# Performance work log

Measured on AMD Instinct MI355X. Metric: run time of the kernel, lower is better.

The kernel has to match this reference:

```python
import jax, jax.numpy as jnp
import numpy as np

N_NODES = 50
VOCAB = 21128
EPS = 1e-8


def _gcn(x, edge_index, W, b):
    # x: [N,128], edge_index: [2,E] (src,dst). PyG GCNConv with self-loops and
    # symmetric normalization: out = D^-1/2 (A+I) D^-1/2 (x W) + b
    N = x.shape[0]
    loops = jnp.arange(N, dtype=edge_index.dtype)
    src = jnp.concatenate([edge_index[0], loops])
    dst = jnp.concatenate([edge_index[1], loops])
    xw = x @ W  # [N,10]
    deg = jax.ops.segment_sum(jnp.ones(src.shape[0], x.dtype), dst, num_segments=N)
    dinv = jnp.where(deg > 0, jax.lax.rsqrt(deg), 0.0)
    norm = dinv[src] * dinv[dst]  # [E+N]
    out = jax.ops.segment_sum(norm[:, None] * xw[src], dst, num_segments=N)
    return out + b


def _mp_match(self_feat, cross_feat, assign_w, w1, b1, w2, b2):
    # cosine similarity along feature dim (torch dim=1), eps-clamped norms
    a = assign_w * self_feat   # [50,10]
    c = assign_w * cross_feat  # [50,10]
    dot = jnp.sum(a * c, axis=1)
    na = jnp.maximum(jnp.linalg.norm(a, axis=1), EPS)
    nc = jnp.maximum(jnp.linalg.norm(c, axis=1), EPS)
    dist = dot / (na * nc)  # [50]
    h = jnp.concatenate([dist[:, None], self_feat], axis=-1)  # [50,11]
    h = jax.nn.relu(h @ w1 + b1) @ w2 + b2  # [50,20]
    return h


def _forward_one(emb_table, conv_w, conv_b, cross_w, attn_coef, assign_w,
                 mp_w1, mp_b1, mp_w2, mp_b2, ffn_w1, ffn_b1, ffn_w2, ffn_b2,
                 u_tok, r_tok, u_edge, r_edge):
    u_emb = emb_table[u_tok]  # [50,128]
    r_emb = emb_table[r_tok]
    u_self = _gcn(u_emb, u_edge, conv_w, conv_b)  # [50,10]
    r_self = _gcn(r_emb, r_edge, conv_w, conv_b)
    u_cross = attn_coef @ (r_emb @ cross_w)  # [50,10]
    r_cross = attn_coef @ (u_emb @ cross_w)
    hu = _mp_match(u_self, u_cross, assign_w, mp_w1, mp_b1, mp_w2, mp_b2)
    hr = _mp_match(r_self, r_cross, assign_w, mp_w1, mp_b1, mp_w2, mp_b2)
    g_u = jnp.max(hu, axis=0)  # [20]
    g_r = jnp.max(hr, axis=0)
    feat = jnp.concatenate([g_u, g_r, g_u * g_r, jnp.abs(g_u - g_r)], axis=-1)  # [80]
    logits = jax.nn.relu(feat @ ffn_w1 + ffn_b1) @ ffn_w2 + ffn_b2  # [1]
    return jax.nn.sigmoid(logits)


def setup_inputs() -> dict:
    key = jax.random.key(0)
    ks = jax.random.split(key, 20)
    B, E, D = 4096, 256, 128
    inp = {
        'utterance_input': jax.random.randint(ks[0], (B, N_NODES), 0, VOCAB, dtype=jnp.int32),
        'response_input': jax.random.randint(ks[1], (B, N_NODES), 0, VOCAB, dtype=jnp.int32),
        'utterance_graph_adj': jax.random.randint(ks[2], (B, 2, E), 0, N_NODES, dtype=jnp.int32),
        'response_graph_adj': jax.random.randint(ks[3], (B, 2, E), 0, N_NODES, dtype=jnp.int32),
        'emb_table': jax.random.normal(ks[4], (VOCAB, D), jnp.float32) * 0.02,
        'conv_w': jax.random.normal(ks[5], (D, 10), jnp.float32) * 0.1,
        'conv_b': jnp.zeros((10,), jnp.float32),
        'cross_w': jax.random.uniform(ks[6], (D, 10), jnp.float32),
        'attn_coef': jax.random.uniform(ks[7], (N_NODES, N_NODES), jnp.float32),
        'assign_w': jax.random.uniform(ks[8], (N_NODES, 10), jnp.float32),
        'mp_w1': jax.random.normal(ks[9], (11, 20), jnp.float32) * 0.3,
        'mp_b1': jnp.zeros((20,), jnp.float32),
        'mp_w2': jax.random.normal(ks[10], (20, 20), jnp.float32) * 0.2,
        'mp_b2': jnp.zeros((20,), jnp.float32),
        'ffn_w1': jax.random.normal(ks[11], (80, 40), jnp.float32) * 0.1,
        'ffn_b1': jnp.zeros((40,), jnp.float32),
        'ffn_w2': jax.random.normal(ks[12], (40, 1), jnp.float32) * 0.1,
        'ffn_b2': jnp.zeros((1,), jnp.float32),
    }
    return inp


def reference(utterance_input, response_input, utterance_graph_adj, response_graph_adj,
              emb_table, conv_w, conv_b, cross_w, attn_coef, assign_w,
              mp_w1, mp_b1, mp_w2, mp_b2, ffn_w1, ffn_b1, ffn_w2, ffn_b2):
    f = jax.vmap(_forward_one,
                 in_axes=(None,) * 14 + (0, 0, 0, 0))
    return f(emb_table, conv_w, conv_b, cross_w, attn_coef, assign_w,
             mp_w1, mp_b1, mp_w2, mp_b2, ffn_w1, ffn_b1, ffn_w2, ffn_b2,
             utterance_input, response_input, utterance_graph_adj, response_graph_adj)  # [B,1]
```

## Files before the change

kernel.cpp:

```cpp
#include <hip/hip_runtime.h>
#include <math.h>

#define NN 50
#define XS 12
#define AWW 13

__global__ __launch_bounds__(256) void precompute_proj(
    const float* __restrict__ emb,
    const float* __restrict__ conv_w,
    const float* __restrict__ cross_w,
    const float* __restrict__ attn,
    float* __restrict__ emb_proj,
    float* __restrict__ attn_t,
    int nrows)
{
    if (blockIdx.x == 0) {
        for (int i = threadIdx.x; i < NN * NN; i += 256) {
            int k = i / NN, r = i % NN;
            attn_t[k * NN + r] = attn[r * NN + k];
        }
    }
    const int lane = threadIdx.x & 63;
    const int w    = threadIdx.x >> 6;
    const int r    = blockIdx.x * 64 + lane;
    if (r >= nrows) return;

    const float* wb = (w < 2) ? conv_w : cross_w;
    const int j0 = (w & 1) * 5;

    float acc[5] = {0.0f, 0.0f, 0.0f, 0.0f, 0.0f};
    const float4* rp = (const float4*)(emb + (size_t)r * 128);
#pragma unroll
    for (int q = 0; q < 32; ++q) {
        float4 v = rp[q];
        const float xs[4] = { v.x, v.y, v.z, v.w };
#pragma unroll
        for (int t = 0; t < 4; ++t) {
            const int k = 4 * q + t;
#pragma unroll
            for (int jj = 0; jj < 5; ++jj)
                acc[jj] += xs[t] * wb[k * 10 + j0 + jj];
        }
    }
    float* op = emb_proj + (size_t)r * 20 + w * 5;
#pragma unroll
    for (int jj = 0; jj < 5; ++jj) op[jj] = acc[jj];
}

__global__ __launch_bounds__(128, 8) void gmn_fused(
    const int* __restrict__ tok_u_all, const int* __restrict__ tok_r_all,
    const int* __restrict__ adj_u_all, const int* __restrict__ adj_r_all,
    const float* __restrict__ emb_proj,
    const float* __restrict__ attn_t,
    const float* __restrict__ conv_b,
    const float* __restrict__ assign_w,
    const float* __restrict__ mp_w1, const float* __restrict__ mp_b1,
    const float* __restrict__ mp_w2, const float* __restrict__ mp_b2,
    const float* __restrict__ ffn_w1, const float* __restrict__ ffn_b1,
    const float* __restrict__ ffn_w2, const float* __restrict__ ffn_b2,
    float* __restrict__ out, int E)
{
    const int b    = blockIdx.x;
    const int tid  = threadIdx.x;
    const int lane = tid & 63;
    const int g    = tid >> 6;

    __shared__ __attribute__((aligned(16))) unsigned s_A[2][NN * AWW];
    __shared__ __attribute__((aligned(16))) float    s_buf[2][NN * XS];
    __shared__ __attribute__((aligned(16))) float    s_g2[2][24];

    for (int i = lane; i < NN * AWW; i += 64) s_A[g][i] = 0u;

    float rx[10];
#pragma unroll
    for (int j = 0; j < 10; ++j) rx[j] = 0.0f;

    if (lane < NN) {
        const int t = (g ? tok_r_all : tok_u_all)[(size_t)b * NN + lane];
        const float4* p = (const float4*)(emb_proj + (size_t)t * 20);
        float4 v0 = p[0], v1 = p[1], v2 = p[2], v3 = p[3], v4 = p[4];
        rx[0] = v0.x; rx[1] = v0.y; rx[2] = v0.z; rx[3] = v0.w;
        rx[4] = v1.x; rx[5] = v1.y; rx[6] = v1.z; rx[7] = v1.w;
        rx[8] = v2.x; rx[9] = v2.y;
        float* ci = &s_buf[g][lane * XS];
        *(float4*)(ci)     = make_float4(v2.z, v2.w, v3.x, v3.y);
        *(float4*)(ci + 4) = make_float4(v3.z, v3.w, v4.x, v4.y);
        *(float2*)(ci + 8) = make_float2(v4.z, v4.w);
    }
    {
        const int* adj = (g ? adj_r_all : adj_u_all) + (size_t)b * 2 * E;
        for (int e = lane; e < E; e += 64) {
            int src = adj[e], dst = adj[E + e];
            atomicAdd(&s_A[g][dst * AWW + (src >> 2)], 1u << ((src & 3) * 8));
        }
    }
    __syncthreads();

    float di = 0.0f;
    float cr[10];
#pragma unroll
    for (int j = 0; j < 10; ++j) cr[j] = 0.0f;

    if (lane < NN) {
        unsigned s = 0;
#pragma unroll
        for (int kw = 0; kw < AWW; ++kw) {
            unsigned a = s_A[g][lane * AWW + kw];
            s += (a & 0xFFu) + ((a >> 8) & 0xFFu) + ((a >> 16) & 0xFFu) + (a >> 24);
        }
        di = rsqrtf(1.0f + (float)s);
#pragma unroll
        for (int j = 0; j < 10; ++j) rx[j] *= di;

        const int i = lane;
        const float* cio = s_buf[g ^ 1];
#pragma unroll 10
        for (int k = 0; k < NN; ++k) {
            float aik = attn_t[k * NN + i];
            const float* crow = &cio[k * XS];
            float4 c0 = *(const float4*)crow;
            float4 c1 = *(const float4*)(crow + 4);
            float2 c2 = *(const float2*)(crow + 8);
            cr[0] += aik * c0.x; cr[1] += aik * c0.y;
            cr[2] += aik * c0.z; cr[3] += aik * c0.w;
            cr[4] += aik * c1.x; cr[5] += aik * c1.y;
            cr[6] += aik * c1.z; cr[7] += aik * c1.w;
            cr[8] += aik * c2.x; cr[9] += aik * c2.y;
        }
    }
    __syncthreads();

    if (lane < NN) {
        float* x = &s_buf[g][lane * XS];
        *(float4*)(x)     = make_float4(rx[0], rx[1], rx[2], rx[3]);
        *(float4*)(x + 4) = make_float4(rx[4], rx[5], rx[6], rx[7]);
        *(float2*)(x + 8) = make_float2(rx[8], rx[9]);
    }
    __builtin_amdgcn_wave_barrier();

    float sf[10];
    float h1[20];

    if (lane < NN) {
        const int i = lane;
        float acc[10];
#pragma unroll
        for (int j = 0; j < 10; ++j) acc[j] = rx[j];
#pragma unroll
        for (int kw = 0; kw < 12; ++kw) {
            unsigned a = s_A[g][i * AWW + kw];
            float cc[4] = { (float)(a & 0xFFu), (float)((a >> 8) & 0xFFu),
                            (float)((a >> 16) & 0xFFu), (float)(a >> 24) };
            const float* x0 = &s_buf[g][(4 * kw) * XS];
#pragma unroll
            for (int t = 0; t < 4; ++t) {
                const float c = cc[t];
                const float* xr = x0 + t * XS;
                float4 p0 = *(const float4*)xr;
                float4 p1 = *(const float4*)(xr + 4);
                float2 p2 = *(const float2*)(xr + 8);
                acc[0] += c * p0.x; acc[1] += c * p0.y;
                acc[2] += c * p0.z; acc[3] += c * p0.w;
                acc[4] += c * p1.x; acc[5] += c * p1.y;
                acc[6] += c * p1.z; acc[7] += c * p1.w;
                acc[8] += c * p2.x; acc[9] += c * p2.y;
            }
        }
        {
            unsigned a = s_A[g][i * AWW + 12];
            float cc[2] = { (float)(a & 0xFFu), (float)((a >> 8) & 0xFFu) };
            const float* x0 = &s_buf[g][48 * XS];
#pragma unroll
            for (int t = 0; t < 2; ++t) {
                const float c = cc[t];
                const float* xr = x0 + t * XS;
                float4 p0 = *(const float4*)xr;
                float4 p1 = *(const float4*)(xr + 4);
                float2 p2 = *(const float2*)(xr + 8);
                acc[0] += c * p0.x; acc[1] += c * p0.y;
                acc[2] += c * p0.z; acc[3] += c * p0.w;
                acc[4] += c * p1.x; acc[5] += c * p1.y;
                acc[6] += c * p1.z; acc[7] += c * p1.w;
                acc[8] += c * p2.x; acc[9] += c * p2.y;
            }
        }
#pragma unroll
        for (int j = 0; j < 10; ++j) sf[j] = di * acc[j] + conv_b[j];

        float dot = 0.0f, na2 = 0.0f, nc2 = 0.0f;
        const float2* awp = (const float2*)(assign_w + i * 10);
#pragma unroll
        for (int q = 0; q < 5; ++q) {
            float2 wv = awp[q];
            float a0 = wv.x * sf[2 * q],     d0 = wv.x * cr[2 * q];
            float a1 = wv.y * sf[2 * q + 1], d1 = wv.y * cr[2 * q + 1];
            dot += a0 * d0 + a1 * d1;
            na2 += a0 * a0 + a1 * a1;
            nc2 += d0 * d0 + d1 * d1;
        }
        float dist = dot / (fmaxf(sqrtf(na2), 1e-8f) * fmaxf(sqrtf(nc2), 1e-8f));

#pragma unroll
        for (int o = 0; o < 20; ++o) {
            float t = mp_b1[o] + dist * mp_w1[o];
#pragma unroll
            for (int j = 0; j < 10; ++j) t += sf[j] * mp_w1[(1 + j) * 20 + o];
            h1[o] = fmaxf(t, 0.0f);
        }
    }

#pragma unroll
    for (int o = 0; o < 20; ++o) {
        float v = -INFINITY;
        if (lane < NN) {
            float t = mp_b2[o];
#pragma unroll
            for (int q = 0; q < 20; ++q) t += h1[q] * mp_w2[q * 20 + o];
            v = t;
        }
        v = fmaxf(v, __shfl_xor(v, 1));
        v = fmaxf(v, __shfl_xor(v, 2));
        v = fmaxf(v, __shfl_xor(v, 4));
        v = fmaxf(v, __shfl_xor(v, 8));
        v = fmaxf(v, __shfl_xor(v, 16));
        v = fmaxf(v, __shfl_xor(v, 32));
        if (lane == 0) s_g2[g][o] = v;
    }
    __syncthreads();

    if (g == 0) {
        float p = 0.0f;
        if (lane < 40) {
            float acc = ffn_b1[lane];
#pragma unroll
            for (int i = 0; i < 20; ++i) {
                float gu = s_g2[0][i], gr = s_g2[1][i];
                acc += gu * ffn_w1[i * 40 + lane]
                     + gr * ffn_w1[(20 + i) * 40 + lane]
                     + gu * gr * ffn_w1[(40 + i) * 40 + lane]
                     + fabsf(gu - gr) * ffn_w1[(60 + i) * 40 + lane];
            }
            p = fmaxf(acc, 0.0f) * ffn_w2[lane];
        }
        p += __shfl_xor(p, 1);  p += __shfl_xor(p, 2);  p += __shfl_xor(p, 4);
        p += __shfl_xor(p, 8);  p += __shfl_xor(p, 16); p += __shfl_xor(p, 32);
        if (lane == 0)
            out[b] = 1.0f / (1.0f + expf(-(p + ffn_b2[0])));
    }
}

extern "C" void kernel_launch(void* const* d_in, const int* in_sizes, int n_in,
                              void* d_out, int out_size, void* d_ws, size_t ws_size,
                              hipStream_t stream)
{
    const int*   tok_u    = (const int*)d_in[0];
    const int*   tok_r    = (const int*)d_in[1];
    const int*   adj_u    = (const int*)d_in[2];
    const int*   adj_r    = (const int*)d_in[3];
    const float* emb      = (const float*)d_in[4];
    const float* conv_w   = (const float*)d_in[5];
    const float* conv_b   = (const float*)d_in[6];
    const float* cross_w  = (const float*)d_in[7];
    const float* attn     = (const float*)d_in[8];
    const float* assign_w = (const float*)d_in[9];
    const float* mp_w1    = (const float*)d_in[10];
    const float* mp_b1    = (const float*)d_in[11];
    const float* mp_w2    = (const float*)d_in[12];
    const float* mp_b2    = (const float*)d_in[13];
    const float* ffn_w1   = (const float*)d_in[14];
    const float* ffn_b1   = (const float*)d_in[15];
    const float* ffn_w2   = (const float*)d_in[16];
    const float* ffn_b2   = (const float*)d_in[17];

    const int B     = in_sizes[0] / 50;
    const int E     = in_sizes[2] / (2 * B);
    const int nrows = in_sizes[4] / 128;

    float* emb_proj = (float*)d_ws;
    float* attn_t   = emb_proj + (size_t)nrows * 20;

    precompute_proj<<<(nrows + 63) / 64, 256, 0, stream>>>(
        emb, conv_w, cross_w, attn, emb_proj, attn_t, nrows);

    gmn_fused<<<B, 128, 0, stream>>>(
        tok_u, tok_r, adj_u, adj_r, emb_proj, attn_t, conv_b,
        assign_w, mp_w1, mp_b1, mp_w2, mp_b2,
        ffn_w1, ffn_b1, ffn_w2, ffn_b2,
        (float*)d_out, E);
}
```

Baseline: 191.1 us.

## Broadcast node features with readlane instead of LDS and drop a barrier

The cross-attention matmul and the GCN neighbour aggregation now broadcast each node's feature row from registers with amdgcn readlane, instead of staging rows in shared memory and reading them back. Each wave computes the cross features from its own embeddings and writes them into the other wave's shared slot. It also reads its adjacency row right after its own atomics, without a block barrier. This cuts LDS traffic and one of the two __syncthreads, at the cost of scalar readlane instructions and more VGPRs. It also relies on ordering of LDS operations within a single wave.

```diff
diff --git a/kernel.cpp b/kernel.cpp
--- a/kernel.cpp
+++ b/kernel.cpp
@@ -4,6 +4,10 @@
 #define NN 50
 #define XS 12
 #define AWW 13
+
+__device__ __forceinline__ float rlane(float v, int k) {
+    return __uint_as_float(__builtin_amdgcn_readlane(__float_as_uint(v), (unsigned)k));
+}
 
 __global__ __launch_bounds__(256) void precompute_proj(
     const float* __restrict__ emb,
@@ -66,14 +70,14 @@
     const int g    = tid >> 6;
 
     __shared__ __attribute__((aligned(16))) unsigned s_A[2][NN * AWW];
-    __shared__ __attribute__((aligned(16))) float    s_buf[2][NN * XS];
+    __shared__ __attribute__((aligned(16))) float    s_x[2][NN * XS];
     __shared__ __attribute__((aligned(16))) float    s_g2[2][24];
 
     for (int i = lane; i < NN * AWW; i += 64) s_A[g][i] = 0u;
 
-    float rx[10];
-#pragma unroll
-    for (int j = 0; j < 10; ++j) rx[j] = 0.0f;
+    float rx[10], ci[10];
+#pragma unroll
+    for (int j = 0; j < 10; ++j) { rx[j] = 0.0f; ci[j] = 0.0f; }
 
     if (lane < NN) {
         const int t = (g ? tok_r_all : tok_u_all)[(size_t)b * NN + lane];
@@ -82,10 +86,9 @@
         rx[0] = v0.x; rx[1] = v0.y; rx[2] = v0.z; rx[3] = v0.w;
         rx[4] = v1.x; rx[5] = v1.y; rx[6] = v1.z; rx[7] = v1.w;
         rx[8] = v2.x; rx[9] = v2.y;
-        float* ci = &s_buf[g][lane * XS];
-        *(float4*)(ci)     = make_float4(v2.z, v2.w, v3.x, v3.y);
-        *(float4*)(ci + 4) = make_float4(v3.z, v3.w, v4.x, v4.y);
-        *(float2*)(ci + 8) = make_float2(v4.z, v4.w);
+        ci[0] = v2.z; ci[1] = v2.w; ci[2] = v3.x; ci[3] = v3.y;
+        ci[4] = v3.z; ci[5] = v3.w; ci[6] = v4.x; ci[7] = v4.y;
+        ci[8] = v4.z; ci[9] = v4.w;
     }
     {
         const int* adj = (g ? adj_r_all : adj_u_all) + (size_t)b * 2 * E;
@@ -94,98 +97,70 @@
             atomicAdd(&s_A[g][dst * AWW + (src >> 2)], 1u << ((src & 3) * 8));
         }
     }
-    __syncthreads();
-
-    float di = 0.0f;
-    float cr[10];
-#pragma unroll
-    for (int j = 0; j < 10; ++j) cr[j] = 0.0f;
-
-    if (lane < NN) {
-        unsigned s = 0;
-#pragma unroll
-        for (int kw = 0; kw < AWW; ++kw) {
-            unsigned a = s_A[g][lane * AWW + kw];
-            s += (a & 0xFFu) + ((a >> 8) & 0xFFu) + ((a >> 16) & 0xFFu) + (a >> 24);
-        }
-        di = rsqrtf(1.0f + (float)s);
-#pragma unroll
-        for (int j = 0; j < 10; ++j) rx[j] *= di;
-
+
+    unsigned arow[AWW];
+    const int rowbase = (lane < NN ? lane : 0) * AWW;
+    unsigned ssum = 0;
+#pragma unroll
+    for (int kw = 0; kw < AWW; ++kw) {
+        unsigned a = s_A[g][rowbase + kw];
+        arow[kw] = a;
+        ssum += (a & 0xFFu) + ((a >> 8) & 0xFFu) + ((a >> 16) & 0xFFu) + (a >> 24);
+    }
+    const float di = rsqrtf(1.0f + (float)ssum);
+#pragma unroll
+    for (int j = 0; j < 10; ++j) rx[j] *= di;
+
+    if (lane < NN) {
         const int i = lane;
-        const float* cio = s_buf[g ^ 1];
-#pragma unroll 10
+        float cr[10];
+#pragma unroll
+        for (int j = 0; j < 10; ++j) cr[j] = 0.0f;
+#pragma unroll 5
         for (int k = 0; k < NN; ++k) {
             float aik = attn_t[k * NN + i];
-            const float* crow = &cio[k * XS];
-            float4 c0 = *(const float4*)crow;
-            float4 c1 = *(const float4*)(crow + 4);
-            float2 c2 = *(const float2*)(crow + 8);
-            cr[0] += aik * c0.x; cr[1] += aik * c0.y;
-            cr[2] += aik * c0.z; cr[3] += aik * c0.w;
-            cr[4] += aik * c1.x; cr[5] += aik * c1.y;
-            cr[6] += aik * c1.z; cr[7] += aik * c1.w;
-            cr[8] += aik * c2.x; cr[9] += aik * c2.y;
-        }
-    }
-    __syncthreads();
-
-    if (lane < NN) {
-        float* x = &s_buf[g][lane * XS];
-        *(float4*)(x)     = make_float4(rx[0], rx[1], rx[2], rx[3]);
-        *(float4*)(x + 4) = make_float4(rx[4], rx[5], rx[6], rx[7]);
-        *(float2*)(x + 8) = make_float2(rx[8], rx[9]);
-    }
-    __builtin_amdgcn_wave_barrier();
+#pragma unroll
+            for (int j = 0; j < 10; ++j)
+                cr[j] += aik * rlane(ci[j], k);
+        }
+        float* cw = &s_x[g ^ 1][i * XS];
+        *(float4*)(cw)     = make_float4(cr[0], cr[1], cr[2], cr[3]);
+        *(float4*)(cw + 4) = make_float4(cr[4], cr[5], cr[6], cr[7]);
+        *(float2*)(cw + 8) = make_float2(cr[8], cr[9]);
+    }
 
     float sf[10];
     float h1[20];
+    if (lane < NN) {
+        float acc[10];
+#pragma unroll
+        for (int j = 0; j < 10; ++j) acc[j] = rx[j];
+#pragma unroll
+        for (int kw = 0; kw < AWW; ++kw) {
+            unsigned a = arow[kw];
+#pragma unroll
+            for (int t = 0; t < 4; ++t) {
+                const int k = 4 * kw + t;
+                if (k >= NN) break;
+                float c = (float)((a >> (8 * t)) & 0xFFu);
+#pragma unroll
+                for (int j = 0; j < 10; ++j)
+                    acc[j] += c * rlane(rx[j], k);
+            }
+        }
+#pragma unroll
+        for (int j = 0; j < 10; ++j) sf[j] = di * acc[j] + conv_b[j];
+    }
+    __syncthreads();
 
     if (lane < NN) {
         const int i = lane;
-        float acc[10];
-#pragma unroll
-        for (int j = 0; j < 10; ++j) acc[j] = rx[j];
-#pragma unroll
-        for (int kw = 0; kw < 12; ++kw) {
-            unsigned a = s_A[g][i * AWW + kw];
-            float cc[4] = { (float)(a & 0xFFu), (float)((a >> 8) & 0xFFu),
-                            (float)((a >> 16) & 0xFFu), (float)(a >> 24) };
-            const float* x0 = &s_buf[g][(4 * kw) * XS];
-#pragma unroll
-            for (int t = 0; t < 4; ++t) {
-                const float c = cc[t];
-                const float* xr = x0 + t * XS;
-                float4 p0 = *(const float4*)xr;
-                float4 p1 = *(const float4*)(xr + 4);
-                float2 p2 = *(const float2*)(xr + 8);
-                acc[0] += c * p0.x; acc[1] += c * p0.y;
-                acc[2] += c * p0.z; acc[3] += c * p0.w;
-                acc[4] += c * p1.x; acc[5] += c * p1.y;
-                acc[6] += c * p1.z; acc[7] += c * p1.w;
-                acc[8] += c * p2.x; acc[9] += c * p2.y;
-            }
-        }
-        {
-            unsigned a = s_A[g][i * AWW + 12];
-            float cc[2] = { (float)(a & 0xFFu), (float)((a >> 8) & 0xFFu) };
-            const float* x0 = &s_buf[g][48 * XS];
-#pragma unroll
-            for (int t = 0; t < 2; ++t) {
-                const float c = cc[t];
-                const float* xr = x0 + t * XS;
-                float4 p0 = *(const float4*)xr;
-                float4 p1 = *(const float4*)(xr + 4);
-                float2 p2 = *(const float2*)(xr + 8);
-                acc[0] += c * p0.x; acc[1] += c * p0.y;
-                acc[2] += c * p0.z; acc[3] += c * p0.w;
-                acc[4] += c * p1.x; acc[5] += c * p1.y;
-                acc[6] += c * p1.z; acc[7] += c * p1.w;
-                acc[8] += c * p2.x; acc[9] += c * p2.y;
-            }
-        }
-#pragma unroll
-        for (int j = 0; j < 10; ++j) sf[j] = di * acc[j] + conv_b[j];
+        const float* cp = &s_x[g][i * XS];
+        float4 c0 = *(const float4*)cp;
+        float4 c1 = *(const float4*)(cp + 4);
+        float2 c2 = *(const float2*)(cp + 8);
+        const float cr[10] = { c0.x, c0.y, c0.z, c0.w,
+                               c1.x, c1.y, c1.z, c1.w, c2.x, c2.y };
 
         float dot = 0.0f, na2 = 0.0f, nc2 = 0.0f;
         const float2* awp = (const float2*)(assign_w + i * 10);
```

After: 206.4 us. +8.0%, slower.
